# Optimization experiments

Measured on AMD Instinct MI355X. Metric: run time of the kernel, lower is better.

Reference implementation:

```python
import jax, jax.numpy as jnp
import numpy as np

N_HEADS = 16
NEG_FILL = -1000000000.0  # masked_fill value from the torch module
PADDING = 0.0             # default padding arg


def setup_inputs() -> dict:
    key = jax.random.key(0)
    kq, kk, kv = jax.random.split(key, 3)
    B, S, D = 2, 2048, 1024
    q = jax.random.normal(kq, (B, S, D), dtype=jnp.float32)
    k = jax.random.normal(kk, (B, S, D), dtype=jnp.float32)
    v = jax.random.normal(kv, (B, S, D), dtype=jnp.float32)
    return {"q": q, "k": k, "v": v, "is_masked": 1}


def reference(q, k, v, is_masked):
    B, S, D = q.shape
    d_key = D // N_HEADS

    def split_heads(x):  # [B,S,D] -> [B,H,S,d_key]
        return x.reshape(B, S, N_HEADS, d_key).transpose(0, 2, 1, 3)

    qh, kh, vh = split_heads(q), split_heads(k), split_heads(v)
    scale = 1.0 / jnp.sqrt(jnp.asarray(d_key, dtype=q.dtype))
    # [B,H,S,S] raw attention scores
    scores = jnp.einsum("bhqd,bhkd->bhqk", qh, kh) * scale
    # value-based mask: keep positions where score != padding
    mask = scores != PADDING
    if is_masked:
        causal = jnp.tril(jnp.ones((S, S), dtype=bool))  # [S,S]
        mask = mask & causal
    scores = jnp.where(mask, scores, jnp.asarray(NEG_FILL, dtype=scores.dtype))
    probs = jax.nn.softmax(scores, axis=-1)
    out = jnp.einsum("bhqk,bhkd->bhqd", probs, vh)  # [B,H,S,d_key]
    return out.transpose(0, 2, 1, 3).reshape(B, S, D)
```

## Files before the change

### kernel.cpp

```cpp
#include <hip/hip_runtime.h>
#include <hip/hip_bf16.h>
#include <math.h>

typedef __bf16 bf16x8 __attribute__((ext_vector_type(8)));
typedef float f32x4 __attribute__((ext_vector_type(4)));

#define S_LEN 2048
#define D_MODEL 1024
#define LT 72
#define CEXP 0.18033688011112042f

__device__ __forceinline__ float fast_exp2(float x) {
    return __builtin_amdgcn_exp2f(x);
}

__device__ __forceinline__ void softsync() {
    asm volatile("s_waitcnt lgkmcnt(0)" ::: "memory");
    __builtin_amdgcn_s_barrier();
    __builtin_amdgcn_sched_barrier(0);
}

template<bool BF>
__device__ __forceinline__ void body(
    const void* __restrict__ qv, const void* __restrict__ kv,
    const void* __restrict__ vv, void* __restrict__ outv,
    int maskflag, int z, int bh,
    __bf16* Ks0, __bf16* Ks1, __bf16* Vt, __bf16* Ps)
{
    const int b    = bh >> 4;
    const int h    = bh & 15;
    const int t    = threadIdx.x;
    const int w    = t >> 6;
    const int lane = t & 63;
    const int m16  = lane & 15;
    const int quad = lane >> 4;

    const int q0 = z * 64;
    const size_t head_off = (size_t)b * S_LEN * D_MODEL + (size_t)h * 64;

    const __bf16* qb = (const __bf16*)qv; const float* qf = (const float*)qv;
    const __bf16* kb = (const __bf16*)kv; const float* kf = (const float*)kv;
    const __bf16* vb = (const __bf16*)vv; const float* vf = (const float*)vv;

    bf16x8 aq0, aq1;
    {
        const int r = q0 + w * 16 + m16;
        if (BF) {
            const __bf16* p = qb + head_off + (size_t)r * D_MODEL;
            aq0 = *(const bf16x8*)&p[quad * 8];
            aq1 = *(const bf16x8*)&p[32 + quad * 8];
        } else {
            const float* p = qf + head_off + (size_t)r * D_MODEL;
            #pragma unroll
            for (int half = 0; half < 2; ++half) {
                float4 x0 = *(const float4*)&p[half * 32 + quad * 8];
                float4 x1 = *(const float4*)&p[half * 32 + quad * 8 + 4];
                bf16x8 f = { (__bf16)x0.x, (__bf16)x0.y, (__bf16)x0.z, (__bf16)x0.w,
                             (__bf16)x1.x, (__bf16)x1.y, (__bf16)x1.z, (__bf16)x1.w };
                if (half == 0) aq0 = f; else aq1 = f;
            }
        }
    }

    f32x4 o[4];
    #pragma unroll
    for (int i = 0; i < 4; ++i) o[i] = (f32x4){0.f,0.f,0.f,0.f};
    float lsum = 0.f;

    const int kg = t >> 4, dg = t & 15;
    const int k0 = kg * 4, d0 = dg * 4;
    const int cst = k0 ^ ((dg & 7) << 3);

    const int ktmax = maskflag ? z : (S_LEN / 64 - 1);

    float4 kr[4], vr[4];
    auto pref = [&](int kt) {
        if (BF) {
            const __bf16* base = kb + head_off + (size_t)kt * 64 * D_MODEL;
            #pragma unroll
            for (int i = 0; i < 2; ++i) {
                int c = t + i * 256, row = c >> 3, off = (c & 7) << 3;
                *(uint4*)&kr[i] = *(const uint4*)&base[(size_t)row * D_MODEL + off];
            }
            const __bf16* vp = vb + head_off + (size_t)(kt * 64 + k0) * D_MODEL + d0;
            #pragma unroll
            for (int j = 0; j < 4; ++j)
                *(uint2*)&vr[j] = *(const uint2*)&vp[(size_t)j * D_MODEL];
        } else {
            const float* base = kf + head_off + (size_t)kt * 64 * D_MODEL;
            #pragma unroll
            for (int i = 0; i < 4; ++i) {
                int c = t + i * 256, row = c >> 4, off = (c & 15) << 2;
                kr[i] = *(const float4*)&base[(size_t)row * D_MODEL + off];
            }
            const float* vp = vf + head_off + (size_t)(kt * 64 + k0) * D_MODEL + d0;
            #pragma unroll
            for (int j = 0; j < 4; ++j)
                vr[j] = *(const float4*)&vp[(size_t)j * D_MODEL];
        }
    };
    auto stageK = [&](__bf16* Ks) {
        if (BF) {
            #pragma unroll
            for (int i = 0; i < 2; ++i) {
                int c = t + i * 256, row = c >> 3, off = (c & 7) << 3;
                *(uint4*)&Ks[row * LT + off] = *(const uint4*)&kr[i];
            }
        } else {
            #pragma unroll
            for (int i = 0; i < 4; ++i) {
                int c = t + i * 256, row = c >> 4, off = (c & 15) << 2;
                float4 ld = kr[i];
                __bf16 pk[4] = { (__bf16)ld.x, (__bf16)ld.y, (__bf16)ld.z, (__bf16)ld.w };
                *(uint2*)&Ks[row * LT + off] = *(uint2*)pk;
            }
        }
    };
    auto stageV = [&]() {
        if (BF) {
            union { uint2 u; __bf16 hh[4]; } r[4];
            #pragma unroll
            for (int j = 0; j < 4; ++j) r[j].u = *(const uint2*)&vr[j];
            #pragma unroll
            for (int j = 0; j < 4; ++j) {
                __bf16 pk[4] = { r[0].hh[j], r[1].hh[j], r[2].hh[j], r[3].hh[j] };
                *(uint2*)&Vt[(d0 + j) * LT + cst] = *(uint2*)pk;
            }
        } else {
            #pragma unroll
            for (int j = 0; j < 4; ++j) {
                __bf16 pk[4] = { (__bf16)vr[0][j], (__bf16)vr[1][j],
                                 (__bf16)vr[2][j], (__bf16)vr[3][j] };
                *(uint2*)&Vt[(d0 + j) * LT + cst] = *(uint2*)pk;
            }
        }
    };

    pref(0);
    for (int kt = 0; kt <= ktmax; ++kt) {
        __bf16* Ks = (kt & 1) ? Ks1 : Ks0;
        stageK(Ks);
        softsync();
        stageV();
        if (kt < ktmax) pref(kt + 1);

        bf16x8 bk0[4], bk1[4];
        #pragma unroll
        for (int nt = 0; nt < 4; ++nt) {
            bk0[nt] = *(bf16x8*)&Ks[(nt * 16 + m16) * LT + quad * 8];
            bk1[nt] = *(bf16x8*)&Ks[(nt * 16 + m16) * LT + 32 + quad * 8];
        }

        f32x4 s[4];
        __builtin_amdgcn_s_setprio(1);
        #pragma unroll
        for (int nt = 0; nt < 4; ++nt) {
            f32x4 acc = (f32x4){0.f,0.f,0.f,0.f};
            acc = __builtin_amdgcn_mfma_f32_16x16x32_bf16(bk0[nt], aq0, acc, 0, 0, 0);
            acc = __builtin_amdgcn_mfma_f32_16x16x32_bf16(bk1[nt], aq1, acc, 0, 0, 0);
            s[nt] = acc;
        }
        __builtin_amdgcn_s_setprio(0);

        const bool diag = maskflag && (kt == z);
        const int qloc = w * 16 + m16;
        float lacc0 = 0.f, lacc1 = 0.f;
        #pragma unroll
        for (int nt = 0; nt < 4; ++nt) {
            union { uint2 u; __bf16 hh[4]; } pk;
            float ps[4];
            #pragma unroll
            for (int reg = 0; reg < 4; ++reg) {
                float raw = s[nt][reg];
                bool valid = (raw != 0.0f);
                if (diag) valid = valid && ((nt * 16 + quad * 4 + reg) <= qloc);
                float p = valid ? fast_exp2(raw * CEXP) : 0.0f;
                ps[reg] = p;
                pk.hh[reg] = (__bf16)p;
            }
            if (nt & 1) lacc1 += (ps[0] + ps[1]) + (ps[2] + ps[3]);
            else        lacc0 += (ps[0] + ps[1]) + (ps[2] + ps[3]);
            *(uint2*)&Ps[(w * 16 + m16) * LT + nt * 16 + quad * 4] = pk.u;
        }
        lsum += lacc0 + lacc1;

        bf16x8 ap0 = *(bf16x8*)&Ps[(w * 16 + m16) * LT + quad * 8];
        bf16x8 ap1 = *(bf16x8*)&Ps[(w * 16 + m16) * LT + 32 + quad * 8];

        softsync();

        bf16x8 bv0[4], bv1[4];
        #pragma unroll
        for (int dt = 0; dt < 4; ++dt) {
            int dim = dt * 16 + m16;
            int sw = ((dim >> 2) & 7) << 3;
            bv0[dt] = *(bf16x8*)&Vt[dim * LT + ((quad * 8) ^ sw)];
            bv1[dt] = *(bf16x8*)&Vt[dim * LT + ((quad * 8 + 32) ^ sw)];
        }

        __builtin_amdgcn_s_setprio(1);
        #pragma unroll
        for (int dt = 0; dt < 4; ++dt) {
            o[dt] = __builtin_amdgcn_mfma_f32_16x16x32_bf16(ap0, bv0[dt], o[dt], 0, 0, 0);
            o[dt] = __builtin_amdgcn_mfma_f32_16x16x32_bf16(ap1, bv1[dt], o[dt], 0, 0, 0);
        }
        __builtin_amdgcn_s_setprio(0);
    }

    float l = lsum;
    l += __shfl_xor(l, 16, 64);
    l += __shfl_xor(l, 32, 64);
    #pragma unroll
    for (int reg = 0; reg < 4; ++reg) {
        float li = __shfl(l, quad * 4 + reg, 64);
        float invl = 1.0f / li;
        int srow = q0 + w * 16 + quad * 4 + reg;
        #pragma unroll
        for (int dt = 0; dt < 4; ++dt) {
            size_t idx = head_off + (size_t)srow * D_MODEL + dt * 16 + m16;
            float val = o[dt][reg] * invl;
            if (BF) ((__bf16*)outv)[idx] = (__bf16)val;
            else    ((float*)outv)[idx]  = val;
        }
    }
}

__global__ __launch_bounds__(256, 4)
void mha_flash_kernel(const void* __restrict__ qv,
                      const void* __restrict__ kv,
                      const void* __restrict__ vv,
                      const int* __restrict__ is_masked_p,
                      void* __restrict__ outv)
{
    __shared__ __attribute__((aligned(16))) __bf16 Ks0[64 * LT];
    __shared__ __attribute__((aligned(16))) __bf16 Ks1[64 * LT];
    __shared__ __attribute__((aligned(16))) __bf16 Vt [64 * LT];
    __shared__ __attribute__((aligned(16))) __bf16 Ps [64 * LT];

    const int id  = blockIdx.x;
    const int xcd = id & 7;
    const int r   = id >> 3;
    const int g   = r >> 2;
    const int z   = (g < 16) ? (31 - g) : (g - 16);
    const int bh  = xcd * 4 + (r & 3);

    const int maskflag = *is_masked_p;

    const __bf16* qprobe = (const __bf16*)qv;
    float px = (float)qprobe[2 * (threadIdx.x & 63)];
    bool okp = (px == px) && (fabsf(px) > 1e-6f) && (fabsf(px) < 100.0f);
    unsigned long long bal = __ballot(okp);
    const bool isbf16 = (__popcll(bal) >= 48);

    if (isbf16)
        body<true >(qv, kv, vv, outv, maskflag, z, bh, Ks0, Ks1, Vt, Ps);
    else
        body<false>(qv, kv, vv, outv, maskflag, z, bh, Ks0, Ks1, Vt, Ps);
}

extern "C" void kernel_launch(void* const* d_in, const int* in_sizes, int n_in,
                              void* d_out, int out_size, void* d_ws, size_t ws_size,
                              hipStream_t stream) {
    const int* is_masked = (const int*)d_in[3];
    mha_flash_kernel<<<dim3(1024), 256, 0, stream>>>(d_in[0], d_in[1], d_in[2], is_masked, d_out);
}
```

Before: 126.2 us.

## Keep P in registers and double-buffer V to drop second barrier

The probability tile is no longer written to shared memory and read back. The QK^T accumulator layout is reused directly as the A operand of the PV MFMA, with V reads permuted so the k-dimension ordering matches. V is now double-buffered and staged before the single barrier, which removes the second block-wide sync per key tile and the P round trip through LDS. In exchange the V fragment loads become four 8-byte reads instead of two 16-byte reads, and more registers stay live.

```diff
diff --git a/kernel.cpp b/kernel.cpp
--- a/kernel.cpp
+++ b/kernel.cpp
@@ -25,7 +25,7 @@
     const void* __restrict__ qv, const void* __restrict__ kv,
     const void* __restrict__ vv, void* __restrict__ outv,
     int maskflag, int z, int bh,
-    __bf16* Ks0, __bf16* Ks1, __bf16* Vt, __bf16* Ps)
+    __bf16* Ks0, __bf16* Ks1, __bf16* Vt0, __bf16* Vt1)
 {
     const int b    = bh >> 4;
     const int h    = bh & 15;
@@ -116,7 +116,7 @@
             }
         }
     };
-    auto stageV = [&]() {
+    auto stageV = [&](__bf16* Vt) {
         if (BF) {
             union { uint2 u; __bf16 hh[4]; } r[4];
             #pragma unroll
@@ -136,12 +136,15 @@
         }
     };
 
+    const int qloc = w * 16 + m16;
+
     pref(0);
     for (int kt = 0; kt <= ktmax; ++kt) {
         __bf16* Ks = (kt & 1) ? Ks1 : Ks0;
+        __bf16* Vt = (kt & 1) ? Vt1 : Vt0;
         stageK(Ks);
+        stageV(Vt);
         softsync();
-        stageV();
         if (kt < ktmax) pref(kt + 1);
 
         bf16x8 bk0[4], bk1[4];
@@ -149,6 +152,21 @@
         for (int nt = 0; nt < 4; ++nt) {
             bk0[nt] = *(bf16x8*)&Ks[(nt * 16 + m16) * LT + quad * 8];
             bk1[nt] = *(bf16x8*)&Ks[(nt * 16 + m16) * LT + 32 + quad * 8];
+        }
+
+        bf16x8 bv0[4], bv1[4];
+        #pragma unroll
+        for (int dt = 0; dt < 4; ++dt) {
+            int dim = dt * 16 + m16;
+            int sw = ((dim >> 2) & 7) << 3;
+            const __bf16* vrow = &Vt[dim * LT];
+            union { bf16x8 v; uint2 u[2]; } t0, t1;
+            t0.u[0] = *(const uint2*)&vrow[( 0 + quad * 4) ^ sw];
+            t0.u[1] = *(const uint2*)&vrow[(16 + quad * 4) ^ sw];
+            t1.u[0] = *(const uint2*)&vrow[(32 + quad * 4) ^ sw];
+            t1.u[1] = *(const uint2*)&vrow[(48 + quad * 4) ^ sw];
+            bv0[dt] = t0.v;
+            bv1[dt] = t1.v;
         }
 
         f32x4 s[4];
@@ -163,46 +181,26 @@
         __builtin_amdgcn_s_setprio(0);
 
         const bool diag = maskflag && (kt == z);
-        const int qloc = w * 16 + m16;
-        float lacc0 = 0.f, lacc1 = 0.f;
+        union { bf16x8 v; __bf16 e[8]; } a0, a1;
         #pragma unroll
         for (int nt = 0; nt < 4; ++nt) {
-            union { uint2 u; __bf16 hh[4]; } pk;
-            float ps[4];
             #pragma unroll
             for (int reg = 0; reg < 4; ++reg) {
                 float raw = s[nt][reg];
                 bool valid = (raw != 0.0f);
                 if (diag) valid = valid && ((nt * 16 + quad * 4 + reg) <= qloc);
                 float p = valid ? fast_exp2(raw * CEXP) : 0.0f;
-                ps[reg] = p;
-                pk.hh[reg] = (__bf16)p;
-            }
-            if (nt & 1) lacc1 += (ps[0] + ps[1]) + (ps[2] + ps[3]);
-            else        lacc0 += (ps[0] + ps[1]) + (ps[2] + ps[3]);
-            *(uint2*)&Ps[(w * 16 + m16) * LT + nt * 16 + quad * 4] = pk.u;
-        }
-        lsum += lacc0 + lacc1;
-
-        bf16x8 ap0 = *(bf16x8*)&Ps[(w * 16 + m16) * LT + quad * 8];
-        bf16x8 ap1 = *(bf16x8*)&Ps[(w * 16 + m16) * LT + 32 + quad * 8];
-
-        softsync();
-
-        bf16x8 bv0[4], bv1[4];
+                lsum += p;
+                if (nt < 2) a0.e[nt * 4 + reg]       = (__bf16)p;
+                else        a1.e[(nt - 2) * 4 + reg] = (__bf16)p;
+            }
+        }
+
+        __builtin_amdgcn_s_setprio(1);
         #pragma unroll
         for (int dt = 0; dt < 4; ++dt) {
-            int dim = dt * 16 + m16;
-            int sw = ((dim >> 2) & 7) << 3;
-            bv0[dt] = *(bf16x8*)&Vt[dim * LT + ((quad * 8) ^ sw)];
-            bv1[dt] = *(bf16x8*)&Vt[dim * LT + ((quad * 8 + 32) ^ sw)];
-        }
-
-        __builtin_amdgcn_s_setprio(1);
-        #pragma unroll
-        for (int dt = 0; dt < 4; ++dt) {
-            o[dt] = __builtin_amdgcn_mfma_f32_16x16x32_bf16(ap0, bv0[dt], o[dt], 0, 0, 0);
-            o[dt] = __builtin_amdgcn_mfma_f32_16x16x32_bf16(ap1, bv1[dt], o[dt], 0, 0, 0);
+            o[dt] = __builtin_amdgcn_mfma_f32_16x16x32_bf16(a0.v, bv0[dt], o[dt], 0, 0, 0);
+            o[dt] = __builtin_amdgcn_mfma_f32_16x16x32_bf16(a1.v, bv1[dt], o[dt], 0, 0, 0);
         }
         __builtin_amdgcn_s_setprio(0);
     }
@@ -234,8 +232,8 @@
 {
     __shared__ __attribute__((aligned(16))) __bf16 Ks0[64 * LT];
     __shared__ __attribute__((aligned(16))) __bf16 Ks1[64 * LT];
-    __shared__ __attribute__((aligned(16))) __bf16 Vt [64 * LT];
-    __shared__ __attribute__((aligned(16))) __bf16 Ps [64 * LT];
+    __shared__ __attribute__((aligned(16))) __bf16 Vt0[64 * LT];
+    __shared__ __attribute__((aligned(16))) __bf16 Vt1[64 * LT];
 
     const int id  = blockIdx.x;
     const int xcd = id & 7;
@@ -253,9 +251,9 @@
     const bool isbf16 = (__popcll(bal) >= 48);
 
     if (isbf16)
-        body<true >(qv, kv, vv, outv, maskflag, z, bh, Ks0, Ks1, Vt, Ps);
+        body<true >(qv, kv, vv, outv, maskflag, z, bh, Ks0, Ks1, Vt0, Vt1);
     else
-        body<false>(qv, kv, vv, outv, maskflag, z, bh, Ks0, Ks1, Vt, Ps);
+        body<false>(qv, kv, vv, outv, maskflag, z, bh, Ks0, Ks1, Vt0, Vt1);
 }
 
 extern "C" void kernel_launch(void* const* d_in, const int* in_sizes, int n_in,
```

New measurement: 234.3 us. 85.7% more time.

## Split key tile across wave pairs with 512-thread blocks and LDS reduction

Applied to the files above, without the earlier changes.

Doubles the block to 8 waves so that each pair of waves shares a 16-row query slice, with each wave handling half of the 64-key tile for both QK and PV. The partial outputs and row sums are combined through shared memory at the end. Global staging loads are redistributed over 512 threads, and bf16 conversions use the packed v_cvt_pk_bf16_f32 instruction. The aim is more waves in flight to hide latency, at the cost of a final cross-wave reduction with extra barriers and higher register and occupancy pressure from launch_bounds(512,8).

```diff
diff --git a/kernel.cpp b/kernel.cpp
--- a/kernel.cpp
+++ b/kernel.cpp
@@ -12,6 +12,12 @@
 
 __device__ __forceinline__ float fast_exp2(float x) {
     return __builtin_amdgcn_exp2f(x);
+}
+
+__device__ __forceinline__ unsigned int pack_bf16(float a, float b) {
+    unsigned int r;
+    asm("v_cvt_pk_bf16_f32 %0, %1, %2" : "=v"(r) : "v"(a), "v"(b));
+    return r;
 }
 
 __device__ __forceinline__ void softsync() {
@@ -34,6 +40,8 @@
     const int lane = t & 63;
     const int m16  = lane & 15;
     const int quad = lane >> 4;
+    const int qg   = w & 3;
+    const int kh   = w >> 2;
 
     const int q0 = z * 64;
     const size_t head_off = (size_t)b * S_LEN * D_MODEL + (size_t)h * 64;
@@ -44,7 +52,7 @@
 
     bf16x8 aq0, aq1;
     {
-        const int r = q0 + w * 16 + m16;
+        const int r = q0 + qg * 16 + m16;
         if (BF) {
             const __bf16* p = qb + head_off + (size_t)r * D_MODEL;
             aq0 = *(const bf16x8*)&p[quad * 8];
@@ -55,9 +63,12 @@
             for (int half = 0; half < 2; ++half) {
                 float4 x0 = *(const float4*)&p[half * 32 + quad * 8];
                 float4 x1 = *(const float4*)&p[half * 32 + quad * 8 + 4];
-                bf16x8 f = { (__bf16)x0.x, (__bf16)x0.y, (__bf16)x0.z, (__bf16)x0.w,
-                             (__bf16)x1.x, (__bf16)x1.y, (__bf16)x1.z, (__bf16)x1.w };
-                if (half == 0) aq0 = f; else aq1 = f;
+                uint2 lo, hi;
+                lo.x = pack_bf16(x0.x, x0.y); lo.y = pack_bf16(x0.z, x0.w);
+                hi.x = pack_bf16(x1.x, x1.y); hi.y = pack_bf16(x1.z, x1.w);
+                uint4 u; u.x = lo.x; u.y = lo.y; u.z = hi.x; u.w = hi.y;
+                if (half == 0) aq0 = __builtin_bit_cast(bf16x8, u);
+                else           aq1 = __builtin_bit_cast(bf16x8, u);
             }
         }
     }
@@ -67,74 +78,73 @@
     for (int i = 0; i < 4; ++i) o[i] = (f32x4){0.f,0.f,0.f,0.f};
     float lsum = 0.f;
 
-    const int kg = t >> 4, dg = t & 15;
-    const int k0 = kg * 4, d0 = dg * 4;
-    const int cst = k0 ^ ((dg & 7) << 3);
+    const int kg = t >> 5, dg = t & 31;
+    const int k0 = kg * 4, d0 = dg * 2;
+    const int cst = k0 ^ ((((unsigned)d0 >> 2) & 7) << 3);
 
     const int ktmax = maskflag ? z : (S_LEN / 64 - 1);
 
-    float4 kr[4], vr[4];
+    uint4  krb;      unsigned int vrb[4];
+    float4 krf[2];   float2 vrf[4];
     auto pref = [&](int kt) {
         if (BF) {
             const __bf16* base = kb + head_off + (size_t)kt * 64 * D_MODEL;
+            { int row = t >> 3, off = (t & 7) << 3;
+              krb = *(const uint4*)&base[(size_t)row * D_MODEL + off]; }
+            const __bf16* vp = vb + head_off + (size_t)(kt * 64 + k0) * D_MODEL + d0;
+            #pragma unroll
+            for (int j = 0; j < 4; ++j)
+                vrb[j] = *(const unsigned int*)&vp[(size_t)j * D_MODEL];
+        } else {
+            const float* base = kf + head_off + (size_t)kt * 64 * D_MODEL;
             #pragma unroll
             for (int i = 0; i < 2; ++i) {
-                int c = t + i * 256, row = c >> 3, off = (c & 7) << 3;
-                *(uint4*)&kr[i] = *(const uint4*)&base[(size_t)row * D_MODEL + off];
-            }
-            const __bf16* vp = vb + head_off + (size_t)(kt * 64 + k0) * D_MODEL + d0;
+                int c = t + i * 512, row = c >> 4, off = (c & 15) << 2;
+                krf[i] = *(const float4*)&base[(size_t)row * D_MODEL + off];
+            }
+            const float* vp = vf + head_off + (size_t)(kt * 64 + k0) * D_MODEL + d0;
             #pragma unroll
             for (int j = 0; j < 4; ++j)
-                *(uint2*)&vr[j] = *(const uint2*)&vp[(size_t)j * D_MODEL];
-        } else {
-            const float* base = kf + head_off + (size_t)kt * 64 * D_MODEL;
-            #pragma unroll
-            for (int i = 0; i < 4; ++i) {
-                int c = t + i * 256, row = c >> 4, off = (c & 15) << 2;
-                kr[i] = *(const float4*)&base[(size_t)row * D_MODEL + off];
-            }
-            const float* vp = vf + head_off + (size_t)(kt * 64 + k0) * D_MODEL + d0;
-            #pragma unroll
-            for (int j = 0; j < 4; ++j)
-                vr[j] = *(const float4*)&vp[(size_t)j * D_MODEL];
+                vrf[j] = *(const float2*)&vp[(size_t)j * D_MODEL];
         }
     };
     auto stageK = [&](__bf16* Ks) {
         if (BF) {
+            int row = t >> 3, off = (t & 7) << 3;
+            *(uint4*)&Ks[row * LT + off] = krb;
+        } else {
             #pragma unroll
             for (int i = 0; i < 2; ++i) {
-                int c = t + i * 256, row = c >> 3, off = (c & 7) << 3;
-                *(uint4*)&Ks[row * LT + off] = *(const uint4*)&kr[i];
-            }
-        } else {
-            #pragma unroll
-            for (int i = 0; i < 4; ++i) {
-                int c = t + i * 256, row = c >> 4, off = (c & 15) << 2;
-                float4 ld = kr[i];
-                __bf16 pk[4] = { (__bf16)ld.x, (__bf16)ld.y, (__bf16)ld.z, (__bf16)ld.w };
-                *(uint2*)&Ks[row * LT + off] = *(uint2*)pk;
+                int c = t + i * 512, row = c >> 4, off = (c & 15) << 2;
+                uint2 pk;
+                pk.x = pack_bf16(krf[i].x, krf[i].y);
+                pk.y = pack_bf16(krf[i].z, krf[i].w);
+                *(uint2*)&Ks[row * LT + off] = pk;
             }
         }
     };
     auto stageV = [&]() {
         if (BF) {
-            union { uint2 u; __bf16 hh[4]; } r[4];
-            #pragma unroll
-            for (int j = 0; j < 4; ++j) r[j].u = *(const uint2*)&vr[j];
-            #pragma unroll
-            for (int j = 0; j < 4; ++j) {
-                __bf16 pk[4] = { r[0].hh[j], r[1].hh[j], r[2].hh[j], r[3].hh[j] };
-                *(uint2*)&Vt[(d0 + j) * LT + cst] = *(uint2*)pk;
-            }
-        } else {
-            #pragma unroll
-            for (int j = 0; j < 4; ++j) {
-                __bf16 pk[4] = { (__bf16)vr[0][j], (__bf16)vr[1][j],
-                                 (__bf16)vr[2][j], (__bf16)vr[3][j] };
-                *(uint2*)&Vt[(d0 + j) * LT + cst] = *(uint2*)pk;
-            }
+            uint2 lo, hi;
+            lo.x = (vrb[0] & 0xFFFFu) | (vrb[1] << 16);
+            lo.y = (vrb[2] & 0xFFFFu) | (vrb[3] << 16);
+            hi.x = (vrb[0] >> 16) | (vrb[1] & 0xFFFF0000u);
+            hi.y = (vrb[2] >> 16) | (vrb[3] & 0xFFFF0000u);
+            *(uint2*)&Vt[(d0    ) * LT + cst] = lo;
+            *(uint2*)&Vt[(d0 + 1) * LT + cst] = hi;
+        } else {
+            uint2 lo, hi;
+            lo.x = pack_bf16(vrf[0].x, vrf[1].x);
+            lo.y = pack_bf16(vrf[2].x, vrf[3].x);
+            hi.x = pack_bf16(vrf[0].y, vrf[1].y);
+            hi.y = pack_bf16(vrf[2].y, vrf[3].y);
+            *(uint2*)&Vt[(d0    ) * LT + cst] = lo;
+            *(uint2*)&Vt[(d0 + 1) * LT + cst] = hi;
         }
     };
+
+    const int qloc = qg * 16 + m16;
+    const int prow = (qg * 16 + m16) * LT;
 
     pref(0);
     for (int kt = 0; kt <= ktmax; ++kt) {
@@ -144,17 +154,17 @@
         stageV();
         if (kt < ktmax) pref(kt + 1);
 
-        bf16x8 bk0[4], bk1[4];
-        #pragma unroll
-        for (int nt = 0; nt < 4; ++nt) {
-            bk0[nt] = *(bf16x8*)&Ks[(nt * 16 + m16) * LT + quad * 8];
-            bk1[nt] = *(bf16x8*)&Ks[(nt * 16 + m16) * LT + 32 + quad * 8];
-        }
-
-        f32x4 s[4];
+        bf16x8 bk0[2], bk1[2];
+        #pragma unroll
+        for (int nt = 0; nt < 2; ++nt) {
+            bk0[nt] = *(bf16x8*)&Ks[(kh * 32 + nt * 16 + m16) * LT + quad * 8];
+            bk1[nt] = *(bf16x8*)&Ks[(kh * 32 + nt * 16 + m16) * LT + 32 + quad * 8];
+        }
+
+        f32x4 s[2];
         __builtin_amdgcn_s_setprio(1);
         #pragma unroll
-        for (int nt = 0; nt < 4; ++nt) {
+        for (int nt = 0; nt < 2; ++nt) {
             f32x4 acc = (f32x4){0.f,0.f,0.f,0.f};
             acc = __builtin_amdgcn_mfma_f32_16x16x32_bf16(bk0[nt], aq0, acc, 0, 0, 0);
             acc = __builtin_amdgcn_mfma_f32_16x16x32_bf16(bk1[nt], aq1, acc, 0, 0, 0);
@@ -163,46 +173,35 @@
         __builtin_amdgcn_s_setprio(0);
 
         const bool diag = maskflag && (kt == z);
-        const int qloc = w * 16 + m16;
-        float lacc0 = 0.f, lacc1 = 0.f;
-        #pragma unroll
-        for (int nt = 0; nt < 4; ++nt) {
-            union { uint2 u; __bf16 hh[4]; } pk;
-            float ps[4];
+        #pragma unroll
+        for (int nt = 0; nt < 2; ++nt) {
+            float pr[4];
             #pragma unroll
             for (int reg = 0; reg < 4; ++reg) {
                 float raw = s[nt][reg];
                 bool valid = (raw != 0.0f);
-                if (diag) valid = valid && ((nt * 16 + quad * 4 + reg) <= qloc);
+                if (diag) valid = valid && ((kh * 32 + nt * 16 + quad * 4 + reg) <= qloc);
                 float p = valid ? fast_exp2(raw * CEXP) : 0.0f;
-                ps[reg] = p;
-                pk.hh[reg] = (__bf16)p;
-            }
-            if (nt & 1) lacc1 += (ps[0] + ps[1]) + (ps[2] + ps[3]);
-            else        lacc0 += (ps[0] + ps[1]) + (ps[2] + ps[3]);
-            *(uint2*)&Ps[(w * 16 + m16) * LT + nt * 16 + quad * 4] = pk.u;
-        }
-        lsum += lacc0 + lacc1;
-
-        bf16x8 ap0 = *(bf16x8*)&Ps[(w * 16 + m16) * LT + quad * 8];
-        bf16x8 ap1 = *(bf16x8*)&Ps[(w * 16 + m16) * LT + 32 + quad * 8];
+                lsum += p;
+                pr[reg] = p;
+            }
+            uint2 pk;
+            pk.x = pack_bf16(pr[0], pr[1]);
+            pk.y = pack_bf16(pr[2], pr[3]);
+            *(uint2*)&Ps[prow + kh * 32 + nt * 16 + quad * 4] = pk;
+        }
+
+        bf16x8 ap = *(bf16x8*)&Ps[prow + kh * 32 + quad * 8];
 
         softsync();
 
-        bf16x8 bv0[4], bv1[4];
+        __builtin_amdgcn_s_setprio(1);
         #pragma unroll
         for (int dt = 0; dt < 4; ++dt) {
             int dim = dt * 16 + m16;
             int sw = ((dim >> 2) & 7) << 3;
-            bv0[dt] = *(bf16x8*)&Vt[dim * LT + ((quad * 8) ^ sw)];
-            bv1[dt] = *(bf16x8*)&Vt[dim * LT + ((quad * 8 + 32) ^ sw)];
-        }
-
-        __builtin_amdgcn_s_setprio(1);
-        #pragma unroll
-        for (int dt = 0; dt < 4; ++dt) {
-            o[dt] = __builtin_amdgcn_mfma_f32_16x16x32_bf16(ap0, bv0[dt], o[dt], 0, 0, 0);
-            o[dt] = __builtin_amdgcn_mfma_f32_16x16x32_bf16(ap1, bv1[dt], o[dt], 0, 0, 0);
+            bf16x8 bv = *(bf16x8*)&Vt[dim * LT + ((kh * 32 + quad * 8) ^ sw)];
+            o[dt] = __builtin_amdgcn_mfma_f32_16x16x32_bf16(ap, bv, o[dt], 0, 0, 0);
         }
         __builtin_amdgcn_s_setprio(0);
     }
@@ -210,22 +209,46 @@
     float l = lsum;
     l += __shfl_xor(l, 16, 64);
     l += __shfl_xor(l, 32, 64);
+
+    __syncthreads();
+    float* M = (float*)Ks0;
     #pragma unroll
-    for (int reg = 0; reg < 4; ++reg) {
-        float li = __shfl(l, quad * 4 + reg, 64);
-        float invl = 1.0f / li;
-        int srow = q0 + w * 16 + quad * 4 + reg;
-        #pragma unroll
-        for (int dt = 0; dt < 4; ++dt) {
-            size_t idx = head_off + (size_t)srow * D_MODEL + dt * 16 + m16;
-            float val = o[dt][reg] * invl;
-            if (BF) ((__bf16*)outv)[idx] = (__bf16)val;
-            else    ((float*)outv)[idx]  = val;
-        }
+    for (int rr = 0; rr < 2; ++rr) {
+        if ((qg >> 1) == rr && kh == 1) {
+            float* bwr = M + (qg & 1) * 1040;
+            #pragma unroll
+            for (int dt = 0; dt < 4; ++dt)
+                *(f32x4*)&bwr[dt * 256 + lane * 4] = o[dt];
+            if (quad == 0) bwr[1024 + m16] = l;
+        }
+        __syncthreads();
+        if ((qg >> 1) == rr && kh == 0) {
+            float* brd = M + (qg & 1) * 1040;
+            #pragma unroll
+            for (int dt = 0; dt < 4; ++dt) {
+                f32x4 po = *(const f32x4*)&brd[dt * 256 + lane * 4];
+                o[dt] += po;
+            }
+            l += brd[1024 + m16];
+            #pragma unroll
+            for (int reg = 0; reg < 4; ++reg) {
+                float li = __shfl(l, quad * 4 + reg, 64);
+                float invl = 1.0f / li;
+                int srow = q0 + qg * 16 + quad * 4 + reg;
+                #pragma unroll
+                for (int dt = 0; dt < 4; ++dt) {
+                    size_t idx = head_off + (size_t)srow * D_MODEL + dt * 16 + m16;
+                    float val = o[dt][reg] * invl;
+                    if (BF) ((__bf16*)outv)[idx] = (__bf16)val;
+                    else    ((float*)outv)[idx]  = val;
+                }
+            }
+        }
+        __syncthreads();
     }
 }
 
-__global__ __launch_bounds__(256, 4)
+__global__ __launch_bounds__(512, 8)
 void mha_flash_kernel(const void* __restrict__ qv,
                       const void* __restrict__ kv,
                       const void* __restrict__ vv,
@@ -262,5 +285,5 @@
                               void* d_out, int out_size, void* d_ws, size_t ws_size,
                               hipStream_t stream) {
     const int* is_masked = (const int*)d_in[3];
-    mha_flash_kernel<<<dim3(1024), 256, 0, stream>>>(d_in[0], d_in[1], d_in[2], is_masked, d_out);
-}
+    mha_flash_kernel<<<dim3(1024), 512, 0, stream>>>(d_in[0], d_in[1], d_in[2], is_masked, d_out);
+}
```

Result: slower. 266.4 us (+111.1%).
